# Performance work log

Measured on AMD Instinct MI355X. Metric: run time of the kernel, lower is better.

The kernel has to match this reference:

```python
import jax, jax.numpy as jnp
import numpy as np

B, H, W, C = 2, 64, 64, 192
DM = int(2.0 * C)   # d_inner = ssm_ratio * hidden_dim = 384
N = 16              # d_state
R = 12              # dt_rank = ceil(C / 16)
K = 4               # scan directions


def _ln(x, g, b, eps):
    mu = jnp.mean(x, axis=-1, keepdims=True)
    var = jnp.var(x, axis=-1, keepdims=True)
    return (x - mu) * jax.lax.rsqrt(var + eps) * g + b


def setup_inputs() -> dict:
    key = jax.random.key(0)
    ks = jax.random.split(key, 8)
    return {
        "input": jax.random.normal(ks[0], (B, H, W, C), jnp.float32),
        "norm_g": jnp.ones((C,), jnp.float32),
        "norm_b": jnp.zeros((C,), jnp.float32),
        "in_proj_w": jax.random.normal(ks[1], (C, 2 * DM), jnp.float32) * 0.02,
        "conv_w": jax.random.normal(ks[2], (DM, 1, 3, 3), jnp.float32) * 0.1,
        "conv_b": jnp.zeros((DM,), jnp.float32),
        "x_proj_w": jax.random.normal(ks[3], (K, R + 2 * N, DM), jnp.float32) * 0.02,
        "dt_w": jax.random.normal(ks[4], (K, DM, R), jnp.float32) * 0.1,
        "dt_b": jax.random.uniform(ks[5], (K, DM), jnp.float32, -4.0, -2.0),
        "A_logs": jnp.tile(jnp.log(jnp.arange(1, N + 1, dtype=jnp.float32))[None, None, :], (K, DM, 1)),
        "Ds": jnp.ones((K, DM), jnp.float32),
        "out_norm_g": jnp.ones((DM,), jnp.float32),
        "out_norm_b": jnp.zeros((DM,), jnp.float32),
        "out_proj_w": jax.random.normal(ks[6], (DM, C), jnp.float32) * 0.02,
    }


def _selective_scan(us, deltas, A, Bs, Cs):
    # us, deltas: (B,K,D,L); A: (K,D,N); Bs, Cs: (B,K,N,L)
    u_l = jnp.moveaxis(us, -1, 0)       # (L,B,K,D)
    d_l = jnp.moveaxis(deltas, -1, 0)   # (L,B,K,D)
    B_l = jnp.moveaxis(Bs, -1, 0)       # (L,B,K,N)
    C_l = jnp.moveaxis(Cs, -1, 0)       # (L,B,K,N)
    h0 = jnp.zeros(us.shape[:3] + (A.shape[-1],), us.dtype)  # (B,K,D,N)

    def step(h, xs):
        u_t, d_t, b_t, c_t = xs
        dA = jnp.exp(d_t[..., None] * A)                       # (B,K,D,N)
        h = dA * h + (d_t * u_t)[..., None] * b_t[:, :, None, :]
        y = jnp.einsum('bkdn,bkn->bkd', h, c_t)
        return h, y

    _, ys = jax.lax.scan(step, h0, (u_l, d_l, B_l, C_l))
    return jnp.moveaxis(ys, 0, -1)  # (B,K,D,L)


def reference(input, norm_g, norm_b, in_proj_w, conv_w, conv_b, x_proj_w,
              dt_w, dt_b, A_logs, Ds, out_norm_g, out_norm_b, out_proj_w):
    Bz, Hh, Ww, Cc = input.shape
    L = Hh * Ww
    # pre-norm
    xn = _ln(input, norm_g, norm_b, 1e-6)
    # input projection -> x, z
    xz = xn @ in_proj_w                      # (B,H,W,2*DM)
    x, z = jnp.split(xz, 2, axis=-1)
    # depthwise conv + SiLU (channels-first)
    x = jnp.transpose(x, (0, 3, 1, 2))       # (B,DM,H,W)
    Dm = x.shape[1]
    x = jax.lax.conv_general_dilated(
        x, conv_w, (1, 1), 'SAME',
        dimension_numbers=('NCHW', 'OIHW', 'NCHW'),
        feature_group_count=Dm) + conv_b[None, :, None, None]
    x = jax.nn.silu(x)
    # 4-direction cross-scan: hw, wh, and their reverses
    x_flat = x.reshape(Bz, Dm, L)
    x_t = jnp.transpose(x, (0, 1, 3, 2)).reshape(Bz, Dm, L)
    xs = jnp.stack([x_flat, x_t], axis=1)                  # (B,2,DM,L)
    xs = jnp.concatenate([xs, jnp.flip(xs, -1)], axis=1)   # (B,4,DM,L)
    Rr = dt_w.shape[2]
    Nn = A_logs.shape[2]
    x_dbl = jnp.einsum('bkdl,kcd->bkcl', xs, x_proj_w)     # (B,4,R+2N,L)
    dts, Bs, Cs = jnp.split(x_dbl, [Rr, Rr + Nn], axis=2)
    deltas = jax.nn.softplus(
        jnp.einsum('bkrl,kdr->bkdl', dts, dt_w) + dt_b[None, :, :, None])
    A = -jnp.exp(A_logs)                                   # (4,DM,N)
    out_y = _selective_scan(xs, deltas, A, Bs, Cs) + Ds[None, :, :, None] * xs
    # merge the 4 directions back
    inv = jnp.flip(out_y[:, 2:], -1)

    def wh(t):
        return jnp.transpose(t.reshape(Bz, Dm, Ww, Hh), (0, 1, 3, 2)).reshape(Bz, Dm, L)

    y = out_y[:, 0] + inv[:, 0] + wh(out_y[:, 1]) + wh(inv[:, 1])  # (B,DM,L)
    y = jnp.transpose(y, (0, 2, 1))                                # (B,L,DM)
    y = _ln(y, out_norm_g, out_norm_b, 1e-5).reshape(Bz, Hh, Ww, Dm)
    y = y * jax.nn.silu(z)
    out = y @ out_proj_w
    # residual (drop_path=0 -> identity)
    return input + out
```

## Files before the change

kernel.cpp:

```cpp
#include <hip/hip_runtime.h>
#include <hip/hip_bf16.h>


typedef __attribute__((ext_vector_type(8))) short short8;
typedef __attribute__((ext_vector_type(4))) float floatx4;

__global__ __launch_bounds__(256) void k_ln(const float* __restrict__ in,
                                            const float* __restrict__ g,
                                            const float* __restrict__ be,
                                            __hip_bfloat16* __restrict__ out) {
  int row = blockIdx.x * 4 + (threadIdx.x >> 6);
  int lane = threadIdx.x & 63;
  const float* x = in + (long)row * 192;
  float v0 = x[lane], v1 = x[lane + 64], v2 = x[lane + 128];
  float s = v0 + v1 + v2;
  float s2 = v0 * v0 + v1 * v1 + v2 * v2;
  #pragma unroll
  for (int o = 32; o > 0; o >>= 1) { s += __shfl_xor(s, o); s2 += __shfl_xor(s2, o); }
  float mu = s * (1.f / 192.f);
  float var = s2 * (1.f / 192.f) - mu * mu;
  float r = rsqrtf(var + 1e-6f);
  __hip_bfloat16* op = out + (long)row * 192;
  op[lane]       = __float2bfloat16((v0 - mu) * r * g[lane]       + be[lane]);
  op[lane + 64]  = __float2bfloat16((v1 - mu) * r * g[lane + 64]  + be[lane + 64]);
  op[lane + 128] = __float2bfloat16((v2 - mu) * r * g[lane + 128] + be[lane + 128]);
}

__global__ __launch_bounds__(256) void k_packw(const float* __restrict__ ipw,
                                               const float* __restrict__ xpw,
                                               const float* __restrict__ opw,
                                               __hip_bfloat16* __restrict__ Wt1,
                                               __hip_bfloat16* __restrict__ Wt2,
                                               __hip_bfloat16* __restrict__ Wt3) {
  int idx = blockIdx.x * 256 + threadIdx.x;
  if (idx < 147456) {
    int n = idx / 192, k = idx - n * 192;
    Wt1[idx] = __float2bfloat16(ipw[(long)k * 768 + n]);
  } else if (idx < 147456 + 73728) {
    int t = idx - 147456;
    int j = t / 384;
    float v = (j < 176) ? xpw[t] : 0.f;
    Wt2[t] = __float2bfloat16(v);
  } else if (idx < 147456 + 73728 + 73728) {
    int t = idx - 147456 - 73728;
    int n = t / 384, k = t - n * 384;
    Wt3[t] = __float2bfloat16(opw[(long)k * 192 + n]);
  }
}

__device__ __forceinline__ int inv_dir(int k, int p) {
  int pt = ((p & 63) << 6) | (p >> 6);
  if (k == 0) return p;
  if (k == 1) return pt;
  if (k == 2) return 4095 - p;
  return 4095 - pt;
}
__device__ __forceinline__ int dir_pix(int k, int l) { return inv_dir(k, l); }

template <int EPI>
__global__ __launch_bounds__(256) void k_gemm_mfma(const __hip_bfloat16* __restrict__ A,
                                                   const __hip_bfloat16* __restrict__ Bt,
                                                   const float* __restrict__ Res,
                                                   float* __restrict__ Co,
                                                   __hip_bfloat16* __restrict__ CoB,
                                                   __hip_bfloat16* __restrict__ Co2B,
                                                   float* __restrict__ dtsS,
                                                   float* __restrict__ BsS,
                                                   float* __restrict__ CsS,
                                                   int M, int N, int Kk) {
  __shared__ __align__(16) short As[64 * 64];
  __shared__ __align__(16) short Bs[64 * 64];
  int tid = threadIdx.x;
  int wave = tid >> 6, lane = tid & 63;
  int mlane = lane & 15, quad = lane >> 4;
  int row0 = blockIdx.y * 64, col0 = blockIdx.x * 64;
  int wr = wave & 1, wc = wave >> 1;
  floatx4 acc[2][2];
  #pragma unroll
  for (int mi = 0; mi < 2; mi++)
    #pragma unroll
    for (int ni = 0; ni < 2; ni++) acc[mi][ni] = (floatx4){0.f, 0.f, 0.f, 0.f};

  for (int k0 = 0; k0 < Kk; k0 += 64) {
    #pragma unroll
    for (int c = tid; c < 512; c += 256) {
      int r = c >> 3, j = c & 7;
      *(float4*)&As[r * 64 + ((j ^ (r & 7)) << 3)] =
          *(const float4*)&A[(long)(row0 + r) * Kk + k0 + j * 8];
    }
    #pragma unroll
    for (int c = tid; c < 512; c += 256) {
      int r = c >> 3, j = c & 7;
      *(float4*)&Bs[r * 64 + ((j ^ (r & 7)) << 3)] =
          *(const float4*)&Bt[(long)(col0 + r) * Kk + k0 + j * 8];
    }
    __syncthreads();
    short8 af[2][2], bf[2][2];
    #pragma unroll
    for (int mi = 0; mi < 2; mi++) {
      int r = wr * 32 + mi * 16 + mlane;
      #pragma unroll
      for (int kk = 0; kk < 2; kk++) {
        int jx = (kk * 4 + quad) ^ (r & 7);
        af[mi][kk] = *(const short8*)&As[r * 64 + jx * 8];
      }
    }
    #pragma unroll
    for (int ni = 0; ni < 2; ni++) {
      int rn = wc * 32 + ni * 16 + mlane;
      #pragma unroll
      for (int kk = 0; kk < 2; kk++) {
        int jx = (kk * 4 + quad) ^ (rn & 7);
        bf[ni][kk] = *(const short8*)&Bs[rn * 64 + jx * 8];
      }
    }
    #pragma unroll
    for (int kk = 0; kk < 2; kk++)
      #pragma unroll
      for (int mi = 0; mi < 2; mi++)
        #pragma unroll
        for (int ni = 0; ni < 2; ni++)
          acc[mi][ni] = __builtin_amdgcn_mfma_f32_16x16x32_bf16(af[mi][kk], bf[ni][kk],
                                                                acc[mi][ni], 0, 0, 0);
    __syncthreads();
  }
  #pragma unroll
  for (int mi = 0; mi < 2; mi++) {
    #pragma unroll
    for (int ni = 0; ni < 2; ni++) {
      int cc = col0 + wc * 32 + ni * 16 + mlane;
      #pragma unroll
      for (int i = 0; i < 4; i++) {
        int rr = row0 + wr * 32 + mi * 16 + quad * 4 + i;
        float v = acc[mi][ni][i];
        if (EPI == 1) {
          Co[(long)rr * N + cc] = v + Res[(long)rr * N + cc];
        } else if (EPI == 2) {
          if (cc < 384) CoB[(long)rr * 384 + cc] = __float2bfloat16(v);
          else          Co2B[(long)rr * 384 + (cc - 384)] = __float2bfloat16(v);
        } else {
          if (cc < 176) {
            int k4 = (cc >= 132) ? 3 : (cc >= 88) ? 2 : (cc >= 44) ? 1 : 0;
            int c = cc - k4 * 44;
            int b = rr >> 12, p = rr & 4095;
            int l = inv_dir(k4, p);
            long lbase = ((long)((b << 2) + k4) << 12) + l;
            if (c < 12)      dtsS[lbase * 12 + c] = v;
            else if (c < 28) BsS[lbase * 16 + (c - 12)] = v;
            else             CsS[lbase * 16 + (c - 28)] = v;
          }
        }
      }
    }
  }
}

__global__ __launch_bounds__(384) void k_conv(const __hip_bfloat16* __restrict__ xbufB,
                                              const float* __restrict__ cw,
                                              const float* __restrict__ cb,
                                              __hip_bfloat16* __restrict__ xcb) {
  int row = blockIdx.x;
  int b = row >> 12, p = row & 4095;
  int h = p >> 6, w0 = p & 63;
  int d = threadIdx.x;
  float acc = cb[d];
  const float* wt = cw + d * 9;
  #pragma unroll
  for (int dh = -1; dh <= 1; dh++) {
    int hh = h + dh;
    if (hh < 0 || hh > 63) continue;
    #pragma unroll
    for (int dw = -1; dw <= 1; dw++) {
      int ww = w0 + dw;
      if (ww < 0 || ww > 63) continue;
      acc += __bfloat162float(xbufB[((long)(b << 12) + (hh << 6) + ww) * 384 + d])
             * wt[(dh + 1) * 3 + (dw + 1)];
    }
  }
  float sg = 1.f / (1.f + __expf(-acc));
  xcb[(long)row * 384 + d] = __float2bfloat16(acc * sg);
}

__device__ __forceinline__ void pow16(float r, float* pws) {
  pws[0] = r;
  #pragma unroll
  for (int n = 1; n < 16; n++) {
    int m = n + 1, c = (m + 1) / 2, f = m - c;
    pws[n] = pws[c - 1] * pws[f - 1];
  }
}

__global__ __launch_bounds__(384) void k_scan0(
    const float* __restrict__ dtsS, const float* __restrict__ BsS,
    const __hip_bfloat16* __restrict__ xcb,
    const float* __restrict__ A_logs, const float* __restrict__ dt_w,
    const float* __restrict__ dt_b,
    float* __restrict__ Eb, float* __restrict__ Dend) {
  int bid = blockIdx.x;
  int s = bid & 127, bk = bid >> 7;
  int k = bk & 3, b = bk >> 2;
  int d = threadIdx.x;
  float w[12];
  const float* dwp = dt_w + ((long)(k * 384) + d) * 12;
  #pragma unroll
  for (int r = 0; r < 12; r++) w[r] = dwp[r];
  float db = dt_b[k * 384 + d];
  const float* al = A_logs + ((long)(k * 384) + d) * 16;
  bool pw = true;
  float av[16];
  #pragma unroll
  for (int n = 0; n < 16; n++) {
    float a = __expf(al[n]);
    av[n] = -a;
    pw = pw && (fabsf(a - (float)(n + 1)) < 1e-3f);
  }
  float h[16];
  #pragma unroll
  for (int n = 0; n < 16; n++) h[n] = 0.f;
  float cum = 0.f;
  long lb = (long)bk * 4096 + s * 32;
  long bpix = (long)(b << 12);

  if (pw) {
    #pragma unroll 4
    for (int t = 0; t < 32; t++) {
      const float4* dq = (const float4*)(dtsS + (lb + t) * 12);
      float4 q0 = dq[0], q1 = dq[1], q2 = dq[2];
      float x = db + q0.x * w[0] + q0.y * w[1] + q0.z * w[2] + q0.w * w[3]
                   + q1.x * w[4] + q1.y * w[5] + q1.z * w[6] + q1.w * w[7]
                   + q2.x * w[8] + q2.y * w[9] + q2.z * w[10] + q2.w * w[11];
      float e = __expf(x);
      float delta = (x > 15.f) ? x : __logf(1.f + e);
      cum += delta;
      int p = dir_pix(k, s * 32 + t);
      float u = __bfloat162float(xcb[(bpix + p) * 384 + d]);
      float du = delta * u;
      float rr = __builtin_amdgcn_rcpf(1.f + e);
      float pws[16]; pow16(rr, pws);
      const float4* Bq = (const float4*)(BsS + (lb + t) * 16);
      float4 b0 = Bq[0], b1 = Bq[1], b2 = Bq[2], b3 = Bq[3];
      float Bl[16] = {b0.x, b0.y, b0.z, b0.w, b1.x, b1.y, b1.z, b1.w,
                      b2.x, b2.y, b2.z, b2.w, b3.x, b3.y, b3.z, b3.w};
      #pragma unroll
      for (int n = 0; n < 16; n++) h[n] = pws[n] * h[n] + du * Bl[n];
    }
  } else {
    for (int t = 0; t < 32; t++) {
      const float4* dq = (const float4*)(dtsS + (lb + t) * 12);
      float4 q0 = dq[0], q1 = dq[1], q2 = dq[2];
      float x = db + q0.x * w[0] + q0.y * w[1] + q0.z * w[2] + q0.w * w[3]
                   + q1.x * w[4] + q1.y * w[5] + q1.z * w[6] + q1.w * w[7]
                   + q2.x * w[8] + q2.y * w[9] + q2.z * w[10] + q2.w * w[11];
      float e = __expf(x);
      float delta = (x > 15.f) ? x : __logf(1.f + e);
      cum += delta;
      int p = dir_pix(k, s * 32 + t);
      float u = __bfloat162float(xcb[(bpix + p) * 384 + d]);
      float du = delta * u;
      const float4* Bq = (const float4*)(BsS + (lb + t) * 16);
      float4 b0 = Bq[0], b1 = Bq[1], b2 = Bq[2], b3 = Bq[3];
      float Bl[16] = {b0.x, b0.y, b0.z, b0.w, b1.x, b1.y, b1.z, b1.w,
                      b2.x, b2.y, b2.z, b2.w, b3.x, b3.y, b3.z, b3.w};
      #pragma unroll
      for (int n = 0; n < 16; n++) {
        float dA = __expf(delta * av[n]);
        h[n] = dA * h[n] + du * Bl[n];
      }
    }
  }
  long g = (long)bk * 128 + s;
  float* Ep = Eb + g * 6144 + d * 16;
  #pragma unroll
  for (int n = 0; n < 16; n++) Ep[n] = h[n];
  Dend[g * 384 + d] = cum;
}

__global__ __launch_bounds__(256) void k_combine(float* __restrict__ Eb,
                                                 const float* __restrict__ Dend,
                                                 const float* __restrict__ A_logs) {
  int t = blockIdx.x * 256 + threadIdx.x;
  int bk = t / 6144;
  int dn = t - bk * 6144;
  int k = bk & 3;
  int d = dn >> 4;
  float av = -__expf(A_logs[(long)k * 6144 + dn]);
  float h = 0.f;
  long ebase = (long)bk * 128 * 6144 + dn;
  long dbase = (long)bk * 128 * 384 + d;
  for (int s = 0; s < 128; s++) {
    long ei = ebase + (long)s * 6144;
    float e = Eb[ei];
    float cum = Dend[dbase + (long)s * 384];
    Eb[ei] = h;
    h = __expf(av * cum) * h + e;
  }
}

__global__ __launch_bounds__(384) void k_scan1(
    const float* __restrict__ dtsS, const float* __restrict__ BsS,
    const float* __restrict__ CsS, const __hip_bfloat16* __restrict__ xcb,
    const float* __restrict__ A_logs, const float* __restrict__ dt_w,
    const float* __restrict__ dt_b, const float* __restrict__ Eb,
    float* __restrict__ ysum) {
  int bid = blockIdx.x;
  int s = bid & 127, bk = bid >> 7;
  int k = bk & 3, b = bk >> 2;
  int d = threadIdx.x;
  float w[12];
  const float* dwp = dt_w + ((long)(k * 384) + d) * 12;
  #pragma unroll
  for (int r = 0; r < 12; r++) w[r] = dwp[r];
  float db = dt_b[k * 384 + d];
  const float* al = A_logs + ((long)(k * 384) + d) * 16;
  bool pw = true;
  float av[16];
  #pragma unroll
  for (int n = 0; n < 16; n++) {
    float a = __expf(al[n]);
    av[n] = -a;
    pw = pw && (fabsf(a - (float)(n + 1)) < 1e-3f);
  }
  float h[16];
  const float* hp = Eb + ((long)bk * 128 + s) * 6144 + d * 16;
  #pragma unroll
  for (int n = 0; n < 16; n++) h[n] = hp[n];
  long lb = (long)bk * 4096 + s * 32;
  long bpix = (long)(b << 12);

  if (pw) {
    #pragma unroll 4
    for (int t = 0; t < 32; t++) {
      const float4* dq = (const float4*)(dtsS + (lb + t) * 12);
      float4 q0 = dq[0], q1 = dq[1], q2 = dq[2];
      float x = db + q0.x * w[0] + q0.y * w[1] + q0.z * w[2] + q0.w * w[3]
                   + q1.x * w[4] + q1.y * w[5] + q1.z * w[6] + q1.w * w[7]
                   + q2.x * w[8] + q2.y * w[9] + q2.z * w[10] + q2.w * w[11];
      float e = __expf(x);
      float delta = (x > 15.f) ? x : __logf(1.f + e);
      int p = dir_pix(k, s * 32 + t);
      float u = __bfloat162float(xcb[(bpix + p) * 384 + d]);
      float du = delta * u;
      float rr = __builtin_amdgcn_rcpf(1.f + e);
      float pws[16]; pow16(rr, pws);
      const float4* Bq = (const float4*)(BsS + (lb + t) * 16);
      float4 b0 = Bq[0], b1 = Bq[1], b2 = Bq[2], b3 = Bq[3];
      float Bl[16] = {b0.x, b0.y, b0.z, b0.w, b1.x, b1.y, b1.z, b1.w,
                      b2.x, b2.y, b2.z, b2.w, b3.x, b3.y, b3.z, b3.w};
      const float4* Cq = (const float4*)(CsS + (lb + t) * 16);
      float4 c0 = Cq[0], c1 = Cq[1], c2 = Cq[2], c3 = Cq[3];
      float Cl[16] = {c0.x, c0.y, c0.z, c0.w, c1.x, c1.y, c1.z, c1.w,
                      c2.x, c2.y, c2.z, c2.w, c3.x, c3.y, c3.z, c3.w};
      float y = 0.f;
      #pragma unroll
      for (int n = 0; n < 16; n++) { h[n] = pws[n] * h[n] + du * Bl[n]; y += h[n] * Cl[n]; }
      atomicAdd(&ysum[(bpix + p) * 384 + d], y);
    }
  } else {
    for (int t = 0; t < 32; t++) {
      const float4* dq = (const float4*)(dtsS + (lb + t) * 12);
      float4 q0 = dq[0], q1 = dq[1], q2 = dq[2];
      float x = db + q0.x * w[0] + q0.y * w[1] + q0.z * w[2] + q0.w * w[3]
                   + q1.x * w[4] + q1.y * w[5] + q1.z * w[6] + q1.w * w[7]
                   + q2.x * w[8] + q2.y * w[9] + q2.z * w[10] + q2.w * w[11];
      float e = __expf(x);
      float delta = (x > 15.f) ? x : __logf(1.f + e);
      int p = dir_pix(k, s * 32 + t);
      float u = __bfloat162float(xcb[(bpix + p) * 384 + d]);
      float du = delta * u;
      const float4* Bq = (const float4*)(BsS + (lb + t) * 16);
      float4 b0 = Bq[0], b1 = Bq[1], b2 = Bq[2], b3 = Bq[3];
      float Bl[16] = {b0.x, b0.y, b0.z, b0.w, b1.x, b1.y, b1.z, b1.w,
                      b2.x, b2.y, b2.z, b2.w, b3.x, b3.y, b3.z, b3.w};
      const float4* Cq = (const float4*)(CsS + (lb + t) * 16);
      float4 c0 = Cq[0], c1 = Cq[1], c2 = Cq[2], c3 = Cq[3];
      float Cl[16] = {c0.x, c0.y, c0.z, c0.w, c1.x, c1.y, c1.z, c1.w,
                      c2.x, c2.y, c2.z, c2.w, c3.x, c3.y, c3.z, c3.w};
      float y = 0.f;
      #pragma unroll
      for (int n = 0; n < 16; n++) {
        float dA = __expf(delta * av[n]);
        h[n] = dA * h[n] + du * Bl[n];
        y += h[n] * Cl[n];
      }
      atomicAdd(&ysum[(bpix + p) * 384 + d], y);
    }
  }
}

__global__ __launch_bounds__(384) void k_merge(const float* __restrict__ ysum,
                                               const __hip_bfloat16* __restrict__ xcb,
                                               const __hip_bfloat16* __restrict__ zbufB,
                                               const float* __restrict__ Ds,
                                               const float* __restrict__ g,
                                               const float* __restrict__ be,
                                               __hip_bfloat16* __restrict__ yactb) {
  int row = blockIdx.x;
  int d = threadIdx.x;
  float v = ysum[(long)row * 384 + d];
  float sd = Ds[d] + Ds[384 + d] + Ds[768 + d] + Ds[1152 + d];
  v += __bfloat162float(xcb[(long)row * 384 + d]) * sd;
  float s1 = v, s2 = v * v;
  #pragma unroll
  for (int o = 32; o > 0; o >>= 1) { s1 += __shfl_xor(s1, o); s2 += __shfl_xor(s2, o); }
  __shared__ float r1[6], r2[6];
  int wv = threadIdx.x >> 6;
  if ((threadIdx.x & 63) == 0) { r1[wv] = s1; r2[wv] = s2; }
  __syncthreads();
  float S1 = 0.f, S2 = 0.f;
  #pragma unroll
  for (int i = 0; i < 6; i++) { S1 += r1[i]; S2 += r2[i]; }
  float mu = S1 * (1.f / 384.f);
  float var = S2 * (1.f / 384.f) - mu * mu;
  float rr = rsqrtf(var + 1e-5f);
  float yn = (v - mu) * rr * g[d] + be[d];
  float z = __bfloat162float(zbufB[(long)row * 384 + d]);
  float sg = z / (1.f + __expf(-z));
  yactb[(long)row * 384 + d] = __float2bfloat16(yn * sg);
}

extern "C" void kernel_launch(void* const* d_in, const int* in_sizes, int n_in,
                              void* d_out, int out_size, void* d_ws, size_t ws_size,
                              hipStream_t stream) {
  const float* input      = (const float*)d_in[0];
  const float* norm_g     = (const float*)d_in[1];
  const float* norm_b     = (const float*)d_in[2];
  const float* in_proj_w  = (const float*)d_in[3];
  const float* conv_w     = (const float*)d_in[4];
  const float* conv_b     = (const float*)d_in[5];
  const float* x_proj_w   = (const float*)d_in[6];
  const float* dt_w       = (const float*)d_in[7];
  const float* dt_b       = (const float*)d_in[8];
  const float* A_logs     = (const float*)d_in[9];
  const float* Ds         = (const float*)d_in[10];
  const float* out_norm_g = (const float*)d_in[11];
  const float* out_norm_b = (const float*)d_in[12];
  const float* out_proj_w = (const float*)d_in[13];
  float* out = (float*)d_out;

  float* ws = (float*)d_ws;
  long o = 0;
  __hip_bfloat16* xnb   = (__hip_bfloat16*)(ws + o); o += 786432;
  __hip_bfloat16* xbufB = (__hip_bfloat16*)(ws + o); o += 1572864;
  __hip_bfloat16* zbufB = (__hip_bfloat16*)(ws + o); o += 1572864;
  __hip_bfloat16* xcb   = (__hip_bfloat16*)(ws + o); o += 1572864;
  __hip_bfloat16* Wt1   = (__hip_bfloat16*)(ws + o); o += 73728;
  __hip_bfloat16* Wt2   = (__hip_bfloat16*)(ws + o); o += 36864;
  __hip_bfloat16* Wt3   = (__hip_bfloat16*)(ws + o); o += 36864;
  float* dtsS           = ws + o;                    o += 393216;
  float* BsS            = ws + o;                    o += 524288;
  float* CsS            = ws + o;                    o += 524288;
  float* Eb             = ws + o;                    o += 6291456;
  float* Dend           = ws + o;                    o += 393216;
  float* ysum           = ws + o;                    o += 3145728;
  __hip_bfloat16* yactb = (__hip_bfloat16*)(ws + o); o += 1572864;

  k_ln<<<dim3(2048), dim3(256), 0, stream>>>(input, norm_g, norm_b, xnb);
  k_packw<<<dim3(1152), dim3(256), 0, stream>>>(in_proj_w, x_proj_w, out_proj_w, Wt1, Wt2, Wt3);
  k_gemm_mfma<2><<<dim3(12, 128), dim3(256), 0, stream>>>(xnb, Wt1, nullptr, nullptr, xbufB, zbufB,
                                                          nullptr, nullptr, nullptr, 8192, 768, 192);
  k_conv<<<dim3(8192), dim3(384), 0, stream>>>(xbufB, conv_w, conv_b, xcb);
  k_gemm_mfma<3><<<dim3(3, 128), dim3(256), 0, stream>>>(xcb, Wt2, nullptr, nullptr, nullptr, nullptr,
                                                         dtsS, BsS, CsS, 8192, 192, 384);
  k_scan0<<<dim3(1024), dim3(384), 0, stream>>>(dtsS, BsS, xcb, A_logs, dt_w, dt_b, Eb, Dend);
  k_combine<<<dim3(192), dim3(256), 0, stream>>>(Eb, Dend, A_logs);
  hipMemsetAsync(ysum, 0, 3145728 * sizeof(float), stream);
  k_scan1<<<dim3(1024), dim3(384), 0, stream>>>(dtsS, BsS, CsS, xcb, A_logs, dt_w, dt_b, Eb, ysum);
  k_merge<<<dim3(8192), dim3(384), 0, stream>>>(ysum, xcb, zbufB, Ds, out_norm_g, out_norm_b, yactb);
  k_gemm_mfma<1><<<dim3(3, 128), dim3(256), 0, stream>>>(yactb, Wt3, input, out, nullptr, nullptr,
                                                         nullptr, nullptr, nullptr, 8192, 192, 384);
}
```

Baseline: 270.2 us.

## Fuse LN with weight packing, fold ysum zeroing into scan, pack scan math

Merges the layernorm and weight-packing kernels into one launch, and replaces the ysum memset with zeroing done inside k_scan0. The scan recurrences are rewritten with float2 pairs so the compiler can emit packed FMA and multiply instructions. k_combine now writes prefix states to a separate Hb buffer instead of rewriting Eb in place, and uses 64-thread blocks across more blocks to spread the serial per-chunk loop over more CUs. This adds another 24 MB workspace buffer and extra write traffic.

```diff
diff --git a/kernel.cpp b/kernel.cpp
--- a/kernel.cpp
+++ b/kernel.cpp
@@ -5,46 +5,55 @@
 typedef __attribute__((ext_vector_type(8))) short short8;
 typedef __attribute__((ext_vector_type(4))) float floatx4;
 
-__global__ __launch_bounds__(256) void k_ln(const float* __restrict__ in,
-                                            const float* __restrict__ g,
-                                            const float* __restrict__ be,
-                                            __hip_bfloat16* __restrict__ out) {
-  int row = blockIdx.x * 4 + (threadIdx.x >> 6);
-  int lane = threadIdx.x & 63;
-  const float* x = in + (long)row * 192;
-  float v0 = x[lane], v1 = x[lane + 64], v2 = x[lane + 128];
-  float s = v0 + v1 + v2;
-  float s2 = v0 * v0 + v1 * v1 + v2 * v2;
-  #pragma unroll
-  for (int o = 32; o > 0; o >>= 1) { s += __shfl_xor(s, o); s2 += __shfl_xor(s2, o); }
-  float mu = s * (1.f / 192.f);
-  float var = s2 * (1.f / 192.f) - mu * mu;
-  float r = rsqrtf(var + 1e-6f);
-  __hip_bfloat16* op = out + (long)row * 192;
-  op[lane]       = __float2bfloat16((v0 - mu) * r * g[lane]       + be[lane]);
-  op[lane + 64]  = __float2bfloat16((v1 - mu) * r * g[lane + 64]  + be[lane + 64]);
-  op[lane + 128] = __float2bfloat16((v2 - mu) * r * g[lane + 128] + be[lane + 128]);
-}
-
-__global__ __launch_bounds__(256) void k_packw(const float* __restrict__ ipw,
-                                               const float* __restrict__ xpw,
-                                               const float* __restrict__ opw,
-                                               __hip_bfloat16* __restrict__ Wt1,
-                                               __hip_bfloat16* __restrict__ Wt2,
-                                               __hip_bfloat16* __restrict__ Wt3) {
-  int idx = blockIdx.x * 256 + threadIdx.x;
-  if (idx < 147456) {
-    int n = idx / 192, k = idx - n * 192;
-    Wt1[idx] = __float2bfloat16(ipw[(long)k * 768 + n]);
-  } else if (idx < 147456 + 73728) {
-    int t = idx - 147456;
-    int j = t / 384;
-    float v = (j < 176) ? xpw[t] : 0.f;
-    Wt2[t] = __float2bfloat16(v);
-  } else if (idx < 147456 + 73728 + 73728) {
-    int t = idx - 147456 - 73728;
-    int n = t / 384, k = t - n * 384;
-    Wt3[t] = __float2bfloat16(opw[(long)k * 192 + n]);
+__device__ __forceinline__ float2 pk_fma(float2 a, float2 b, float2 c) {
+  return make_float2(fmaf(a.x, b.x, c.x), fmaf(a.y, b.y, c.y));
+}
+__device__ __forceinline__ float2 pk_mul(float2 a, float2 b) {
+  return make_float2(a.x * b.x, a.y * b.y);
+}
+
+__global__ __launch_bounds__(256) void k_ln_packw(const float* __restrict__ in,
+                                                  const float* __restrict__ g,
+                                                  const float* __restrict__ be,
+                                                  const float* __restrict__ ipw,
+                                                  const float* __restrict__ xpw,
+                                                  const float* __restrict__ opw,
+                                                  __hip_bfloat16* __restrict__ xnb,
+                                                  __hip_bfloat16* __restrict__ Wt1,
+                                                  __hip_bfloat16* __restrict__ Wt2,
+                                                  __hip_bfloat16* __restrict__ Wt3) {
+  int bid = blockIdx.x;
+  if (bid < 2048) {
+    int row = bid * 4 + (threadIdx.x >> 6);
+    int lane = threadIdx.x & 63;
+    const float* x = in + (long)row * 192;
+    float v0 = x[lane], v1 = x[lane + 64], v2 = x[lane + 128];
+    float s = v0 + v1 + v2;
+    float s2 = v0 * v0 + v1 * v1 + v2 * v2;
+    #pragma unroll
+    for (int o = 32; o > 0; o >>= 1) { s += __shfl_xor(s, o); s2 += __shfl_xor(s2, o); }
+    float mu = s * (1.f / 192.f);
+    float var = s2 * (1.f / 192.f) - mu * mu;
+    float r = rsqrtf(var + 1e-6f);
+    __hip_bfloat16* op = xnb + (long)row * 192;
+    op[lane]       = __float2bfloat16((v0 - mu) * r * g[lane]       + be[lane]);
+    op[lane + 64]  = __float2bfloat16((v1 - mu) * r * g[lane + 64]  + be[lane + 64]);
+    op[lane + 128] = __float2bfloat16((v2 - mu) * r * g[lane + 128] + be[lane + 128]);
+  } else {
+    int idx = (bid - 2048) * 256 + threadIdx.x;
+    if (idx < 147456) {
+      int n = idx / 192, k = idx - n * 192;
+      Wt1[idx] = __float2bfloat16(ipw[(long)k * 768 + n]);
+    } else if (idx < 147456 + 73728) {
+      int t = idx - 147456;
+      int j = t / 384;
+      float v = (j < 176) ? xpw[t] : 0.f;
+      Wt2[t] = __float2bfloat16(v);
+    } else if (idx < 147456 + 73728 + 73728) {
+      int t = idx - 147456 - 73728;
+      int n = t / 384, k = t - n * 384;
+      Wt3[t] = __float2bfloat16(opw[(long)k * 192 + n]);
+    }
   }
 }
 
@@ -195,8 +204,14 @@
     const __hip_bfloat16* __restrict__ xcb,
     const float* __restrict__ A_logs, const float* __restrict__ dt_w,
     const float* __restrict__ dt_b,
-    float* __restrict__ Eb, float* __restrict__ Dend) {
+    float* __restrict__ Eb, float* __restrict__ Dend,
+    float* __restrict__ ysum) {
   int bid = blockIdx.x;
+  {
+    float4 z4 = {0.f, 0.f, 0.f, 0.f};
+    float4* zp = (float4*)(ysum + (long)bid * 3072) + threadIdx.x;
+    zp[0] = z4; zp[384] = z4;
+  }
   int s = bid & 127, bk = bid >> 7;
   int k = bk & 3, b = bk >> 2;
   int d = threadIdx.x;
@@ -214,14 +229,14 @@
     av[n] = -a;
     pw = pw && (fabsf(a - (float)(n + 1)) < 1e-3f);
   }
-  float h[16];
-  #pragma unroll
-  for (int n = 0; n < 16; n++) h[n] = 0.f;
   float cum = 0.f;
   long lb = (long)bk * 4096 + s * 32;
   long bpix = (long)(b << 12);
 
   if (pw) {
+    float2 h2[8];
+    #pragma unroll
+    for (int i = 0; i < 8; i++) h2[i] = make_float2(0.f, 0.f);
     #pragma unroll 4
     for (int t = 0; t < 32; t++) {
       const float4* dq = (const float4*)(dtsS + (lb + t) * 12);
@@ -235,16 +250,28 @@
       int p = dir_pix(k, s * 32 + t);
       float u = __bfloat162float(xcb[(bpix + p) * 384 + d]);
       float du = delta * u;
+      float2 du2 = make_float2(du, du);
       float rr = __builtin_amdgcn_rcpf(1.f + e);
       float pws[16]; pow16(rr, pws);
       const float4* Bq = (const float4*)(BsS + (lb + t) * 16);
       float4 b0 = Bq[0], b1 = Bq[1], b2 = Bq[2], b3 = Bq[3];
-      float Bl[16] = {b0.x, b0.y, b0.z, b0.w, b1.x, b1.y, b1.z, b1.w,
-                      b2.x, b2.y, b2.z, b2.w, b3.x, b3.y, b3.z, b3.w};
-      #pragma unroll
-      for (int n = 0; n < 16; n++) h[n] = pws[n] * h[n] + du * Bl[n];
-    }
+      float2 B2[8] = {{b0.x, b0.y}, {b0.z, b0.w}, {b1.x, b1.y}, {b1.z, b1.w},
+                      {b2.x, b2.y}, {b2.z, b2.w}, {b3.x, b3.y}, {b3.z, b3.w}};
+      #pragma unroll
+      for (int i = 0; i < 8; i++) {
+        float2 p2 = make_float2(pws[2 * i], pws[2 * i + 1]);
+        h2[i] = pk_fma(du2, B2[i], pk_mul(p2, h2[i]));
+      }
+    }
+    long g = (long)bk * 128 + s;
+    float* Ep = Eb + g * 6144 + d * 16;
+    #pragma unroll
+    for (int i = 0; i < 8; i++) { Ep[2 * i] = h2[i].x; Ep[2 * i + 1] = h2[i].y; }
+    Dend[g * 384 + d] = cum;
   } else {
+    float h[16];
+    #pragma unroll
+    for (int n = 0; n < 16; n++) h[n] = 0.f;
     for (int t = 0; t < 32; t++) {
       const float4* dq = (const float4*)(dtsS + (lb + t) * 12);
       float4 q0 = dq[0], q1 = dq[1], q2 = dq[2];
@@ -267,18 +294,19 @@
         h[n] = dA * h[n] + du * Bl[n];
       }
     }
-  }
-  long g = (long)bk * 128 + s;
-  float* Ep = Eb + g * 6144 + d * 16;
-  #pragma unroll
-  for (int n = 0; n < 16; n++) Ep[n] = h[n];
-  Dend[g * 384 + d] = cum;
-}
-
-__global__ __launch_bounds__(256) void k_combine(float* __restrict__ Eb,
-                                                 const float* __restrict__ Dend,
-                                                 const float* __restrict__ A_logs) {
-  int t = blockIdx.x * 256 + threadIdx.x;
+    long g = (long)bk * 128 + s;
+    float* Ep = Eb + g * 6144 + d * 16;
+    #pragma unroll
+    for (int n = 0; n < 16; n++) Ep[n] = h[n];
+    Dend[g * 384 + d] = cum;
+  }
+}
+
+__global__ __launch_bounds__(64) void k_combine(const float* __restrict__ Eb,
+                                                const float* __restrict__ Dend,
+                                                const float* __restrict__ A_logs,
+                                                float* __restrict__ Hb) {
+  int t = blockIdx.x * 64 + threadIdx.x;
   int bk = t / 6144;
   int dn = t - bk * 6144;
   int k = bk & 3;
@@ -288,11 +316,8 @@
   long ebase = (long)bk * 128 * 6144 + dn;
   long dbase = (long)bk * 128 * 384 + d;
   for (int s = 0; s < 128; s++) {
-    long ei = ebase + (long)s * 6144;
-    float e = Eb[ei];
-    float cum = Dend[dbase + (long)s * 384];
-    Eb[ei] = h;
-    h = __expf(av * cum) * h + e;
+    Hb[ebase + (long)s * 6144] = h;
+    h = __expf(av * Dend[dbase + (long)s * 384]) * h + Eb[ebase + (long)s * 6144];
   }
 }
 
@@ -300,7 +325,7 @@
     const float* __restrict__ dtsS, const float* __restrict__ BsS,
     const float* __restrict__ CsS, const __hip_bfloat16* __restrict__ xcb,
     const float* __restrict__ A_logs, const float* __restrict__ dt_w,
-    const float* __restrict__ dt_b, const float* __restrict__ Eb,
+    const float* __restrict__ dt_b, const float* __restrict__ Hb,
     float* __restrict__ ysum) {
   int bid = blockIdx.x;
   int s = bid & 127, bk = bid >> 7;
@@ -320,14 +345,14 @@
     av[n] = -a;
     pw = pw && (fabsf(a - (float)(n + 1)) < 1e-3f);
   }
-  float h[16];
-  const float* hp = Eb + ((long)bk * 128 + s) * 6144 + d * 16;
-  #pragma unroll
-  for (int n = 0; n < 16; n++) h[n] = hp[n];
   long lb = (long)bk * 4096 + s * 32;
   long bpix = (long)(b << 12);
+  const float* hp = Hb + ((long)bk * 128 + s) * 6144 + d * 16;
 
   if (pw) {
+    float2 h2[8];
+    #pragma unroll
+    for (int i = 0; i < 8; i++) h2[i] = make_float2(hp[2 * i], hp[2 * i + 1]);
     #pragma unroll 4
     for (int t = 0; t < 32; t++) {
       const float4* dq = (const float4*)(dtsS + (lb + t) * 12);
@@ -340,22 +365,30 @@
       int p = dir_pix(k, s * 32 + t);
       float u = __bfloat162float(xcb[(bpix + p) * 384 + d]);
       float du = delta * u;
+      float2 du2 = make_float2(du, du);
       float rr = __builtin_amdgcn_rcpf(1.f + e);
       float pws[16]; pow16(rr, pws);
       const float4* Bq = (const float4*)(BsS + (lb + t) * 16);
       float4 b0 = Bq[0], b1 = Bq[1], b2 = Bq[2], b3 = Bq[3];
-      float Bl[16] = {b0.x, b0.y, b0.z, b0.w, b1.x, b1.y, b1.z, b1.w,
-                      b2.x, b2.y, b2.z, b2.w, b3.x, b3.y, b3.z, b3.w};
+      float2 B2[8] = {{b0.x, b0.y}, {b0.z, b0.w}, {b1.x, b1.y}, {b1.z, b1.w},
+                      {b2.x, b2.y}, {b2.z, b2.w}, {b3.x, b3.y}, {b3.z, b3.w}};
       const float4* Cq = (const float4*)(CsS + (lb + t) * 16);
       float4 c0 = Cq[0], c1 = Cq[1], c2 = Cq[2], c3 = Cq[3];
-      float Cl[16] = {c0.x, c0.y, c0.z, c0.w, c1.x, c1.y, c1.z, c1.w,
-                      c2.x, c2.y, c2.z, c2.w, c3.x, c3.y, c3.z, c3.w};
-      float y = 0.f;
-      #pragma unroll
-      for (int n = 0; n < 16; n++) { h[n] = pws[n] * h[n] + du * Bl[n]; y += h[n] * Cl[n]; }
-      atomicAdd(&ysum[(bpix + p) * 384 + d], y);
+      float2 C2[8] = {{c0.x, c0.y}, {c0.z, c0.w}, {c1.x, c1.y}, {c1.z, c1.w},
+                      {c2.x, c2.y}, {c2.z, c2.w}, {c3.x, c3.y}, {c3.z, c3.w}};
+      float2 y2 = make_float2(0.f, 0.f);
+      #pragma unroll
+      for (int i = 0; i < 8; i++) {
+        float2 p2 = make_float2(pws[2 * i], pws[2 * i + 1]);
+        h2[i] = pk_fma(du2, B2[i], pk_mul(p2, h2[i]));
+        y2 = pk_fma(h2[i], C2[i], y2);
+      }
+      atomicAdd(&ysum[(bpix + p) * 384 + d], y2.x + y2.y);
     }
   } else {
+    float h[16];
+    #pragma unroll
+    for (int n = 0; n < 16; n++) h[n] = hp[n];
     for (int t = 0; t < 32; t++) {
       const float4* dq = (const float4*)(dtsS + (lb + t) * 12);
       float4 q0 = dq[0], q1 = dq[1], q2 = dq[2];
@@ -451,20 +484,21 @@
   float* CsS            = ws + o;                    o += 524288;
   float* Eb             = ws + o;                    o += 6291456;
   float* Dend           = ws + o;                    o += 393216;
+  float* Hb             = ws + o;                    o += 6291456;
   float* ysum           = ws + o;                    o += 3145728;
   __hip_bfloat16* yactb = (__hip_bfloat16*)(ws + o); o += 1572864;
 
-  k_ln<<<dim3(2048), dim3(256), 0, stream>>>(input, norm_g, norm_b, xnb);
-  k_packw<<<dim3(1152), dim3(256), 0, stream>>>(in_proj_w, x_proj_w, out_proj_w, Wt1, Wt2, Wt3);
+  k_ln_packw<<<dim3(3200), dim3(256), 0, stream>>>(input, norm_g, norm_b,
+                                                   in_proj_w, x_proj_w, out_proj_w,
+                                                   xnb, Wt1, Wt2, Wt3);
   k_gemm_mfma<2><<<dim3(12, 128), dim3(256), 0, stream>>>(xnb, Wt1, nullptr, nullptr, xbufB, zbufB,
                                                           nullptr, nullptr, nullptr, 8192, 768, 192);
   k_conv<<<dim3(8192), dim3(384), 0, stream>>>(xbufB, conv_w, conv_b, xcb);
   k_gemm_mfma<3><<<dim3(3, 128), dim3(256), 0, stream>>>(xcb, Wt2, nullptr, nullptr, nullptr, nullptr,
                                                          dtsS, BsS, CsS, 8192, 192, 384);
-  k_scan0<<<dim3(1024), dim3(384), 0, stream>>>(dtsS, BsS, xcb, A_logs, dt_w, dt_b, Eb, Dend);
-  k_combine<<<dim3(192), dim3(256), 0, stream>>>(Eb, Dend, A_logs);
-  hipMemsetAsync(ysum, 0, 3145728 * sizeof(float), stream);
-  k_scan1<<<dim3(1024), dim3(384), 0, stream>>>(dtsS, BsS, CsS, xcb, A_logs, dt_w, dt_b, Eb, ysum);
+  k_scan0<<<dim3(1024), dim3(384), 0, stream>>>(dtsS, BsS, xcb, A_logs, dt_w, dt_b, Eb, Dend, ysum);
+  k_combine<<<dim3(768), dim3(64), 0, stream>>>(Eb, Dend, A_logs, Hb);
+  k_scan1<<<dim3(1024), dim3(384), 0, stream>>>(dtsS, BsS, CsS, xcb, A_logs, dt_w, dt_b, Hb, ysum);
   k_merge<<<dim3(8192), dim3(384), 0, stream>>>(ysum, xcb, zbufB, Ds, out_norm_g, out_norm_b, yactb);
   k_gemm_mfma<1><<<dim3(3, 128), dim3(256), 0, stream>>>(yactb, Wt3, input, out, nullptr, nullptr,
                                                          nullptr, nullptr, nullptr, 8192, 192, 384);
```

Result: slower. 284.7 us (+5.4%).
